# Performance work log

Hardware: AMD Instinct MI355X
Metric: run time of the kernel (lower is better)

## Reference

```python
import jax, jax.numpy as jnp
import numpy as np

NUM_HEADS = 12
HIDDEN = 768
HEAD = HIDDEN // NUM_HEADS
SCALE = HIDDEN ** (-0.5)  # NB: module scales by hidden_dim**-0.5, not head_size**-0.5


def setup_inputs() -> dict:
    key = jax.random.key(0)
    ks = jax.random.split(key, 8)
    B, N = 16, 512
    std = HIDDEN ** (-0.5)
    return {
        "x": jax.random.normal(ks[0], (B, N, HIDDEN), dtype=jnp.float32),
        "encoding_bias": jax.random.normal(ks[1], (B, N, N), dtype=jnp.float32),
        "Wq": jax.random.normal(ks[2], (HIDDEN, HIDDEN), dtype=jnp.float32) * std,
        "Wk": jax.random.normal(ks[3], (HIDDEN, HIDDEN), dtype=jnp.float32) * std,
        "Wv": jax.random.normal(ks[4], (HIDDEN, HIDDEN), dtype=jnp.float32) * std,
        "bv": jax.random.normal(ks[5], (HIDDEN,), dtype=jnp.float32) * 0.01,
        "Wo": jax.random.normal(ks[6], (HIDDEN, HIDDEN), dtype=jnp.float32) * std,
        "bo": jax.random.normal(ks[7], (HIDDEN,), dtype=jnp.float32) * 0.01,
    }


def reference(x, encoding_bias, Wq, Wk, Wv, bv, Wo, bo):
    B, N, _ = x.shape
    # torch nn.Linear: y = x @ W.T (+ b)
    q = (x @ Wq.T).reshape(B, N, NUM_HEADS, HEAD)
    k = (x @ Wk.T).reshape(B, N, NUM_HEADS, HEAD)
    v = (x @ Wv.T + bv).reshape(B, N, NUM_HEADS, HEAD)
    # scores: [B, H, N, N] with additive graph bias broadcast over heads
    a = jnp.einsum("bnhd,bmhd->bhnm", q, k) * SCALE + encoding_bias[:, None, :, :]
    # data-dependent pad mask: rows whose scores are identically zero
    pad_mask = jnp.all(a == 0, axis=-1)  # [B, H, N]
    a = jnp.where(pad_mask[..., None], -jnp.inf, a)
    a = jax.nn.softmax(a, axis=-1)
    a = jnp.nan_to_num(a)  # all -inf rows -> NaN -> 0
    o = jnp.einsum("bhnm,bmhd->bnhd", a, v).reshape(B, N, HIDDEN)
    # dropout is identity in eval mode
    return o @ Wo.T + bo
```

## Files before the change

### kernel.cpp

```cpp
#include <hip/hip_runtime.h>
#include <stdint.h>

typedef unsigned short u16;
typedef unsigned int u32;
typedef __bf16 bf16x8 __attribute__((ext_vector_type(8)));
typedef float f32x4 __attribute__((ext_vector_type(4)));

#define NH 12
#define HD 64
#define SEQ 512
#define BATCH 16
#define HID 768
#define SCALE_Q 0.03608439182435161f

__device__ __forceinline__ u16 f2bf(float f) {
    u32 u = __builtin_bit_cast(u32, f);
    u32 r = (u + 0x7FFFu + ((u >> 16) & 1u)) >> 16;
    return (u16)r;
}
__device__ __forceinline__ float bf2f(u16 h) {
    return __builtin_bit_cast(float, (u32)h << 16);
}

__device__ __forceinline__ void gl2lds16(const u16* g, u16* lds_base) {
    __builtin_amdgcn_global_load_lds(
        (const __attribute__((address_space(1))) u32*)g,
        (__attribute__((address_space(3))) u32*)lds_base, 16, 0, 0);
}

#define NXB 6144
#define NEB 4096
#define NWB 576
__global__ void cvt_all(const float* __restrict__ x, const float* __restrict__ eb,
                        const float* __restrict__ w0, const float* __restrict__ w1,
                        const float* __restrict__ w2, const float* __restrict__ w3,
                        u16* __restrict__ dst) {
    int b = blockIdx.x;
    const float* s; int sb;
    if (b < NXB) { s = x; sb = 0; }
    else if (b < NXB + NEB) { s = eb; sb = NXB; }
    else if (b < NXB + NEB + NWB) { s = w0; sb = NXB + NEB; }
    else if (b < NXB + NEB + 2 * NWB) { s = w1; sb = NXB + NEB + NWB; }
    else if (b < NXB + NEB + 3 * NWB) { s = w2; sb = NXB + NEB + 2 * NWB; }
    else { s = w3; sb = NXB + NEB + 3 * NWB; }
    int li = (b - sb) * 1024 + threadIdx.x * 4;
    float4 v = *(const float4*)(s + li);
    ushort4 o;
    o.x = f2bf(v.x); o.y = f2bf(v.y); o.z = f2bf(v.z); o.w = f2bf(v.w);
    *(ushort4*)(dst + (size_t)b * 1024 + threadIdx.x * 4) = o;
}

__device__ __forceinline__ void stage_gemm(
    const u16* __restrict__ Ag, const u16* __restrict__ Bg, int k0,
    u16* As, u16* Bs, int r0, int q0, int r1, int q1, int w)
{
    gl2lds16(Ag + (size_t)r0 * HID + k0 + q0, As + w * 512);
    gl2lds16(Ag + (size_t)r1 * HID + k0 + q1, As + 2048 + w * 512);
    gl2lds16(Bg + (size_t)r0 * HID + k0 + q0, Bs + w * 512);
    gl2lds16(Bg + (size_t)r1 * HID + k0 + q1, Bs + 2048 + w * 512);
}

__device__ __forceinline__ void gemm_mainloop(
    const u16* __restrict__ Ag, const u16* __restrict__ Bg,
    u16 (*As)[128 * 32], u16 (*Bs)[128 * 32], f32x4 (&acc)[4][4])
{
    const int tid = threadIdx.x;
    const int l = tid & 63, w = tid >> 6;
    const int wm = w & 1, wn = w >> 1;
    const int lr = l & 15, lg = l >> 4;

    const int c0 = tid, c1 = tid + 256;
    const int r0 = c0 >> 2, q0 = (((c0 & 3) ^ ((r0 >> 1) & 3)) * 8);
    const int r1 = c1 >> 2, q1 = (((c1 & 3) ^ ((r1 >> 1) & 3)) * 8);

    const int sA = (lg ^ ((lr >> 1) & 3)) * 8;

    stage_gemm(Ag, Bg, 0, As[0], Bs[0], r0, q0, r1, q1, w);
    stage_gemm(Ag, Bg, 32, As[1], Bs[1], r0, q0, r1, q1, w);

    int cur = 0;
    for (int i = 0; i < 24; i++) {
        if (i < 23)
            asm volatile("s_waitcnt vmcnt(4) lgkmcnt(0)" ::: "memory");
        else
            asm volatile("s_waitcnt vmcnt(0) lgkmcnt(0)" ::: "memory");
        __builtin_amdgcn_s_barrier();
        __builtin_amdgcn_sched_barrier(0);

        int nxt = cur + 2; if (nxt >= 3) nxt -= 3;
        if (i < 22)
            stage_gemm(Ag, Bg, (i + 2) * 32, As[nxt], Bs[nxt], r0, q0, r1, q1, w);

        bf16x8 af[4], bfr[4];
#pragma unroll
        for (int mi = 0; mi < 4; mi++)
            af[mi] = *(const bf16x8*)(As[cur] + (wm * 64 + mi * 16 + lr) * 32 + sA);
#pragma unroll
        for (int ni = 0; ni < 4; ni++)
            bfr[ni] = *(const bf16x8*)(Bs[cur] + (wn * 64 + ni * 16 + lr) * 32 + sA);
#pragma unroll
        for (int mi = 0; mi < 4; mi++)
#pragma unroll
            for (int ni = 0; ni < 4; ni++)
                acc[mi][ni] = __builtin_amdgcn_mfma_f32_16x16x32_bf16(af[mi], bfr[ni], acc[mi][ni], 0, 0, 0);

        cur += 1; if (cur >= 3) cur -= 3;
    }
}

__global__ __launch_bounds__(256, 3) void gemm_qkv(
    const u16* __restrict__ xb, const u16* __restrict__ wq,
    const u16* __restrict__ wk, const u16* __restrict__ wv,
    const float* __restrict__ bv,
    u16* __restrict__ qtb, u16* __restrict__ kb, u16* __restrict__ vtb)
{
    __shared__ __align__(16) u16 As[3][128 * 32];
    __shared__ __align__(16) u16 Bs[3][128 * 32];
    const int tid = threadIdx.x;
    const int l = tid & 63, w = tid >> 6;
    const int wm = w & 1, wn = w >> 1;
    const int lr = l & 15, lg = l >> 4;
    const int mt = blockIdx.x, nt = blockIdx.y, z = blockIdx.z;

    const u16* Bw = (z == 0) ? wq : (z == 1) ? wk : wv;
    const u16* Ag = xb + (size_t)(mt * 128) * HID;
    const u16* Bg = Bw + (size_t)(nt * 128) * HID;

    f32x4 acc[4][4] = {};
    gemm_mainloop(Ag, Bg, As, Bs, acc);

    const float sc = (z == 0) ? SCALE_Q : 1.0f;
#pragma unroll
    for (int mi = 0; mi < 4; mi++) {
#pragma unroll
        for (int ni = 0; ni < 4; ni++) {
            const int jg = nt * 128 + wn * 64 + ni * 16 + lr;
            const int h = jg >> 6, d = jg & 63;
            const int i0 = mt * 128 + wm * 64 + mi * 16 + lg * 4;
            const int b = i0 >> 9, n0 = i0 & 511;
            if (z == 1) {
#pragma unroll
                for (int r2 = 0; r2 < 4; r2++)
                    kb[((size_t)(b * NH + h) * SEQ + n0 + r2) * HD + d] = f2bf(acc[mi][ni][r2]);
            } else {
                float bb = (z == 2) ? bv[jg] : 0.0f;
                ushort4 pk;
                pk.x = f2bf(fmaf(acc[mi][ni][0], sc, bb));
                pk.y = f2bf(fmaf(acc[mi][ni][1], sc, bb));
                pk.z = f2bf(fmaf(acc[mi][ni][2], sc, bb));
                pk.w = f2bf(fmaf(acc[mi][ni][3], sc, bb));
                u16* O = (z == 0) ? qtb : vtb;
                *(ushort4*)(O + ((size_t)(b * NH + h) * HD + d) * SEQ + n0) = pk;
            }
        }
    }
}

__global__ __launch_bounds__(256, 3) void gemm_out(
    const u16* __restrict__ A, const u16* __restrict__ wo,
    const float* __restrict__ bo, float* __restrict__ Cout)
{
    __shared__ __align__(16) u16 As[3][128 * 32];
    __shared__ __align__(16) u16 Bs[3][128 * 32];
    const int tid = threadIdx.x;
    const int l = tid & 63, w = tid >> 6;
    const int wm = w & 1, wn = w >> 1;
    const int lr = l & 15, lg = l >> 4;
    const int mt = blockIdx.x, nt = blockIdx.y;

    const u16* Ag = A + (size_t)(mt * 128) * HID;
    const u16* Bg = wo + (size_t)(nt * 128) * HID;

    f32x4 acc[4][4] = {};
    gemm_mainloop(Ag, Bg, As, Bs, acc);

#pragma unroll
    for (int mi = 0; mi < 4; mi++) {
#pragma unroll
        for (int ni = 0; ni < 4; ni++) {
            const int jg = nt * 128 + wn * 64 + ni * 16 + lr;
            float bb = bo[jg];
#pragma unroll
            for (int r2 = 0; r2 < 4; r2++) {
                int ig = mt * 128 + wm * 64 + mi * 16 + lg * 4 + r2;
                Cout[(size_t)ig * HID + jg] = acc[mi][ni][r2] + bb;
            }
        }
    }
}

__device__ __forceinline__ void stage_kv(
    const u16* __restrict__ Kg, const u16* __restrict__ Vg, int mt0,
    u16* Ksb, u16* Vsb, int kr0, int kc0, int kr1, int kc1, int w)
{
    gl2lds16(Kg + (size_t)(mt0 + kr0) * HD + kc0 * 8, Ksb + w * 512);
    gl2lds16(Kg + (size_t)(mt0 + kr1) * HD + kc1 * 8, Ksb + 2048 + w * 512);
    gl2lds16(Vg + (size_t)kr0 * SEQ + mt0 + kc0 * 8, Vsb + w * 512);
    gl2lds16(Vg + (size_t)kr1 * SEQ + mt0 + kc1 * 8, Vsb + 2048 + w * 512);
}

__global__ __launch_bounds__(256, 4) void attn_kernel(
    const u16* __restrict__ qtb, const u16* __restrict__ kb, const u16* __restrict__ vtb,
    const u16* __restrict__ ebb, u16* __restrict__ ob)
{
    __shared__ __align__(16) u16 Ks[2][64 * 64];
    __shared__ __align__(16) u16 Vs[2][64 * 64];
    __shared__ __align__(16) u16 Ps[4][16 * 64];

    const int tid = threadIdx.x;
    const int l = tid & 63, w = tid >> 6;
    const int lr = l & 15, lg = l >> 4;
    const int h = blockIdx.x, qt = blockIdx.y, b = blockIdx.z;
    const int bh = b * NH + h;
    const int qrow0 = qt * 64 + w * 16;

    const u16* Kg = kb + (size_t)bh * SEQ * HD;
    const u16* Vg = vtb + (size_t)bh * HD * SEQ;
    const u16* Eg = ebb + ((size_t)b * SEQ + qrow0 + lg * 4) * SEQ;

    const int p0 = tid, p1 = tid + 256;
    const int kr0 = p0 >> 3, kc0 = (p0 & 7) ^ (kr0 & 7);
    const int kr1 = p1 >> 3, kc1 = (p1 & 7) ^ (kr1 & 7);

    stage_kv(Kg, Vg, 0, Ks[0], Vs[0], kr0, kc0, kr1, kc1, w);

    const u16* Qg = qtb + (size_t)bh * HD * SEQ + qrow0 + lr;
    bf16x8 qf0, qf1;
#pragma unroll
    for (int j = 0; j < 8; j++) {
        qf0[j] = __builtin_bit_cast(__bf16, Qg[(size_t)(lg * 8 + j) * SEQ]);
        qf1[j] = __builtin_bit_cast(__bf16, Qg[(size_t)(lg * 8 + j + 32) * SEQ]);
    }

    bf16x8 ones;
#pragma unroll
    for (int j = 0; j < 8; j++) ones[j] = __builtin_bit_cast(__bf16, (u16)0x3F80);

    f32x4 oacc[4] = {};
    f32x4 lacc = {};
    float amax[4] = {0.f, 0.f, 0.f, 0.f};

    for (int t = 0; t < 8; t++) {
        const int cur = t & 1;
        const int mt0 = t * 64;
        __syncthreads();

        u16 bl[4][4];
#pragma unroll
        for (int mi = 0; mi < 4; mi++)
#pragma unroll
            for (int r = 0; r < 4; r++)
                bl[mi][r] = Eg[(size_t)r * SEQ + mt0 + mi * 16 + lr];

        if (t < 7)
            stage_kv(Kg, Vg, mt0 + 64, Ks[cur ^ 1], Vs[cur ^ 1], kr0, kc0, kr1, kc1, w);

        float sm[4][4];
#pragma unroll
        for (int mi = 0; mi < 4; mi++) {
            const int row = mi * 16 + lr;
            bf16x8 kf0 = *(const bf16x8*)(Ks[cur] + row * 64 + ((lg ^ (row & 7)) * 8));
            bf16x8 kf1 = *(const bf16x8*)(Ks[cur] + row * 64 + (((4 + lg) ^ (row & 7)) * 8));
            f32x4 s;
#pragma unroll
            for (int r = 0; r < 4; r++) s[r] = bf2f(bl[mi][r]);
            s = __builtin_amdgcn_mfma_f32_16x16x32_bf16(qf0, kf0, s, 0, 0, 0);
            s = __builtin_amdgcn_mfma_f32_16x16x32_bf16(qf1, kf1, s, 0, 0, 0);
#pragma unroll
            for (int r = 0; r < 4; r++) {
                float sv = s[r];
                amax[r] = fmaxf(amax[r], fabsf(sv));
                sm[mi][r] = __expf(sv);
            }
        }

        u16* Pw = Ps[w];
#pragma unroll
        for (int mi = 0; mi < 4; mi++)
#pragma unroll
            for (int r = 0; r < 4; r++) {
                const int q = lg * 4 + r;
                const int chunk = mi * 2 + (lr >> 3);
                Pw[q * 64 + ((chunk ^ (q & 7)) * 8) + (lr & 7)] = f2bf(sm[mi][r]);
            }

#pragma unroll
        for (int ks = 0; ks < 2; ks++) {
            bf16x8 pf = *(const bf16x8*)(Pw + lr * 64 + (((ks * 4 + lg) ^ (lr & 7)) * 8));
#pragma unroll
            for (int di = 0; di < 4; di++) {
                const int row = di * 16 + lr;
                bf16x8 vf = *(const bf16x8*)(Vs[cur] + row * 64 + (((ks * 4 + lg) ^ (row & 7)) * 8));
                oacc[di] = __builtin_amdgcn_mfma_f32_16x16x32_bf16(pf, vf, oacc[di], 0, 0, 0);
            }
            lacc = __builtin_amdgcn_mfma_f32_16x16x32_bf16(pf, ones, lacc, 0, 0, 0);
        }
    }

#pragma unroll
    for (int r = 0; r < 4; r++) {
        float am = amax[r];
        am = fmaxf(am, __shfl_xor(am, 1));
        am = fmaxf(am, __shfl_xor(am, 2));
        am = fmaxf(am, __shfl_xor(am, 4));
        am = fmaxf(am, __shfl_xor(am, 8));
        float inv = (am > 0.f) ? (1.0f / lacc[r]) : 0.0f;
        int n = qrow0 + lg * 4 + r;
        u16* orow = ob + ((size_t)b * SEQ + n) * HID + h * HD;
#pragma unroll
        for (int di = 0; di < 4; di++)
            orow[di * 16 + lr] = f2bf(oacc[di][r] * inv);
    }
}

extern "C" void kernel_launch(void* const* d_in, const int* in_sizes, int n_in,
                              void* d_out, int out_size, void* d_ws, size_t ws_size,
                              hipStream_t stream) {
    (void)in_sizes; (void)n_in; (void)out_size; (void)ws_size;
    const float* x  = (const float*)d_in[0];
    const float* eb = (const float*)d_in[1];
    const float* Wq = (const float*)d_in[2];
    const float* Wk = (const float*)d_in[3];
    const float* Wv = (const float*)d_in[4];
    const float* bv = (const float*)d_in[5];
    const float* Wo = (const float*)d_in[6];
    const float* bo = (const float*)d_in[7];
    float* out = (float*)d_out;

    const int NX = BATCH * SEQ * HID;
    const int NW = HID * HID;
    const int NE = BATCH * SEQ * SEQ;
    u16* ws   = (u16*)d_ws;
    u16* xb   = ws;
    u16* ebb  = xb + NX;
    u16* wqb  = ebb + NE;
    u16* wkb  = wqb + NW;
    u16* wvb  = wkb + NW;
    u16* wob  = wvb + NW;
    u16* qtb  = wob + NW;
    u16* kb   = qtb + NX;
    u16* vtb  = kb + NX;
    u16* obuf = vtb + NX;

    cvt_all<<<NXB + NEB + 4 * NWB, 256, 0, stream>>>(x, eb, Wq, Wk, Wv, Wo, ws);

    gemm_qkv<<<dim3(64, 6, 3), 256, 0, stream>>>(xb, wqb, wkb, wvb, bv, qtb, kb, vtb);

    attn_kernel<<<dim3(NH, 8, BATCH), 256, 0, stream>>>(qtb, kb, vtb, ebb, obuf);

    gemm_out<<<dim3(64, 6), 256, 0, stream>>>(obuf, wob, bo, out);
}
```

Measured before the change: 204.2 us.

## Widen QKV GEMM tile to 128x256 and remap attention blocks per XCD

```diff
diff --git a/kernel.cpp b/kernel.cpp
--- a/kernel.cpp
+++ b/kernel.cpp
@@ -50,38 +50,50 @@
     *(ushort4*)(dst + (size_t)b * 1024 + threadIdx.x * 4) = o;
 }
 
-__device__ __forceinline__ void stage_gemm(
+__device__ __forceinline__ void stage_gemm256(
     const u16* __restrict__ Ag, const u16* __restrict__ Bg, int k0,
-    u16* As, u16* Bs, int r0, int q0, int r1, int q1, int w)
-{
-    gl2lds16(Ag + (size_t)r0 * HID + k0 + q0, As + w * 512);
-    gl2lds16(Ag + (size_t)r1 * HID + k0 + q1, As + 2048 + w * 512);
-    gl2lds16(Bg + (size_t)r0 * HID + k0 + q0, Bs + w * 512);
-    gl2lds16(Bg + (size_t)r1 * HID + k0 + q1, Bs + 2048 + w * 512);
-}
-
-__device__ __forceinline__ void gemm_mainloop(
+    u16* As, u16* Bs,
+    int ra0, int qa0, int ra1, int qa1,
+    int rb0, int qb0, int rb1, int qb1,
+    int rb2, int qb2, int rb3, int qb3, int w)
+{
+    gl2lds16(Ag + (size_t)ra0 * HID + k0 + qa0, As + w * 512);
+    gl2lds16(Ag + (size_t)ra1 * HID + k0 + qa1, As + 2048 + w * 512);
+    gl2lds16(Bg + (size_t)rb0 * HID + k0 + qb0, Bs + w * 512);
+    gl2lds16(Bg + (size_t)rb1 * HID + k0 + qb1, Bs + 2048 + w * 512);
+    gl2lds16(Bg + (size_t)rb2 * HID + k0 + qb2, Bs + 4096 + w * 512);
+    gl2lds16(Bg + (size_t)rb3 * HID + k0 + qb3, Bs + 6144 + w * 512);
+}
+
+__device__ __forceinline__ void gemm_mainloop256(
     const u16* __restrict__ Ag, const u16* __restrict__ Bg,
-    u16 (*As)[128 * 32], u16 (*Bs)[128 * 32], f32x4 (&acc)[4][4])
+    u16 (*As)[128 * 32], u16 (*Bs)[256 * 32], f32x4 (&acc)[4][8])
 {
     const int tid = threadIdx.x;
     const int l = tid & 63, w = tid >> 6;
     const int wm = w & 1, wn = w >> 1;
     const int lr = l & 15, lg = l >> 4;
 
-    const int c0 = tid, c1 = tid + 256;
-    const int r0 = c0 >> 2, q0 = (((c0 & 3) ^ ((r0 >> 1) & 3)) * 8);
-    const int r1 = c1 >> 2, q1 = (((c1 & 3) ^ ((r1 >> 1) & 3)) * 8);
+    const int ca0 = tid, ca1 = tid + 256;
+    const int ra0 = ca0 >> 2, qa0 = (((ca0 & 3) ^ ((ra0 >> 1) & 3)) * 8);
+    const int ra1 = ca1 >> 2, qa1 = (((ca1 & 3) ^ ((ra1 >> 1) & 3)) * 8);
+    const int cb0 = tid, cb1 = tid + 256, cb2 = tid + 512, cb3 = tid + 768;
+    const int rb0 = cb0 >> 2, qb0 = (((cb0 & 3) ^ ((rb0 >> 1) & 3)) * 8);
+    const int rb1 = cb1 >> 2, qb1 = (((cb1 & 3) ^ ((rb1 >> 1) & 3)) * 8);
+    const int rb2 = cb2 >> 2, qb2 = (((cb2 & 3) ^ ((rb2 >> 1) & 3)) * 8);
+    const int rb3 = cb3 >> 2, qb3 = (((cb3 & 3) ^ ((rb3 >> 1) & 3)) * 8);
 
     const int sA = (lg ^ ((lr >> 1) & 3)) * 8;
 
-    stage_gemm(Ag, Bg, 0, As[0], Bs[0], r0, q0, r1, q1, w);
-    stage_gemm(Ag, Bg, 32, As[1], Bs[1], r0, q0, r1, q1, w);
+    stage_gemm256(Ag, Bg, 0, As[0], Bs[0], ra0, qa0, ra1, qa1,
+                  rb0, qb0, rb1, qb1, rb2, qb2, rb3, qb3, w);
+    stage_gemm256(Ag, Bg, 32, As[1], Bs[1], ra0, qa0, ra1, qa1,
+                  rb0, qb0, rb1, qb1, rb2, qb2, rb3, qb3, w);
 
     int cur = 0;
     for (int i = 0; i < 24; i++) {
         if (i < 23)
-            asm volatile("s_waitcnt vmcnt(4) lgkmcnt(0)" ::: "memory");
+            asm volatile("s_waitcnt vmcnt(6) lgkmcnt(0)" ::: "memory");
         else
             asm volatile("s_waitcnt vmcnt(0) lgkmcnt(0)" ::: "memory");
         __builtin_amdgcn_s_barrier();
@@ -89,33 +101,34 @@
 
         int nxt = cur + 2; if (nxt >= 3) nxt -= 3;
         if (i < 22)
-            stage_gemm(Ag, Bg, (i + 2) * 32, As[nxt], Bs[nxt], r0, q0, r1, q1, w);
-
-        bf16x8 af[4], bfr[4];
+            stage_gemm256(Ag, Bg, (i + 2) * 32, As[nxt], Bs[nxt], ra0, qa0, ra1, qa1,
+                          rb0, qb0, rb1, qb1, rb2, qb2, rb3, qb3, w);
+
+        bf16x8 af[4], bfr[8];
 #pragma unroll
         for (int mi = 0; mi < 4; mi++)
             af[mi] = *(const bf16x8*)(As[cur] + (wm * 64 + mi * 16 + lr) * 32 + sA);
 #pragma unroll
-        for (int ni = 0; ni < 4; ni++)
-            bfr[ni] = *(const bf16x8*)(Bs[cur] + (wn * 64 + ni * 16 + lr) * 32 + sA);
-#pragma unroll
-        for (int mi = 0; mi < 4; mi++)
-#pragma unroll
-            for (int ni = 0; ni < 4; ni++)
+        for (int ni = 0; ni < 8; ni++)
+            bfr[ni] = *(const bf16x8*)(Bs[cur] + (wn * 128 + ni * 16 + lr) * 32 + sA);
+#pragma unroll
+        for (int mi = 0; mi < 4; mi++)
+#pragma unroll
+            for (int ni = 0; ni < 8; ni++)
                 acc[mi][ni] = __builtin_amdgcn_mfma_f32_16x16x32_bf16(af[mi], bfr[ni], acc[mi][ni], 0, 0, 0);
 
         cur += 1; if (cur >= 3) cur -= 3;
     }
 }
 
-__global__ __launch_bounds__(256, 3) void gemm_qkv(
+__global__ __launch_bounds__(256, 2) void gemm_qkv(
     const u16* __restrict__ xb, const u16* __restrict__ wq,
     const u16* __restrict__ wk, const u16* __restrict__ wv,
     const float* __restrict__ bv,
     u16* __restrict__ qtb, u16* __restrict__ kb, u16* __restrict__ vtb)
 {
     __shared__ __align__(16) u16 As[3][128 * 32];
-    __shared__ __align__(16) u16 Bs[3][128 * 32];
+    __shared__ __align__(16) u16 Bs[3][256 * 32];
     const int tid = threadIdx.x;
     const int l = tid & 63, w = tid >> 6;
     const int wm = w & 1, wn = w >> 1;
@@ -124,17 +137,17 @@
 
     const u16* Bw = (z == 0) ? wq : (z == 1) ? wk : wv;
     const u16* Ag = xb + (size_t)(mt * 128) * HID;
-    const u16* Bg = Bw + (size_t)(nt * 128) * HID;
-
-    f32x4 acc[4][4] = {};
-    gemm_mainloop(Ag, Bg, As, Bs, acc);
+    const u16* Bg = Bw + (size_t)(nt * 256) * HID;
+
+    f32x4 acc[4][8] = {};
+    gemm_mainloop256(Ag, Bg, As, Bs, acc);
 
     const float sc = (z == 0) ? SCALE_Q : 1.0f;
 #pragma unroll
     for (int mi = 0; mi < 4; mi++) {
 #pragma unroll
-        for (int ni = 0; ni < 4; ni++) {
-            const int jg = nt * 128 + wn * 64 + ni * 16 + lr;
+        for (int ni = 0; ni < 8; ni++) {
+            const int jg = nt * 256 + wn * 128 + ni * 16 + lr;
             const int h = jg >> 6, d = jg & 63;
             const int i0 = mt * 128 + wm * 64 + mi * 16 + lg * 4;
             const int b = i0 >> 9, n0 = i0 & 511;
@@ -156,6 +169,64 @@
     }
 }
 
+__device__ __forceinline__ void stage_gemm(
+    const u16* __restrict__ Ag, const u16* __restrict__ Bg, int k0,
+    u16* As, u16* Bs, int r0, int q0, int r1, int q1, int w)
+{
+    gl2lds16(Ag + (size_t)r0 * HID + k0 + q0, As + w * 512);
+    gl2lds16(Ag + (size_t)r1 * HID + k0 + q1, As + 2048 + w * 512);
+    gl2lds16(Bg + (size_t)r0 * HID + k0 + q0, Bs + w * 512);
+    gl2lds16(Bg + (size_t)r1 * HID + k0 + q1, Bs + 2048 + w * 512);
+}
+
+__device__ __forceinline__ void gemm_mainloop(
+    const u16* __restrict__ Ag, const u16* __restrict__ Bg,
+    u16 (*As)[128 * 32], u16 (*Bs)[128 * 32], f32x4 (&acc)[4][4])
+{
+    const int tid = threadIdx.x;
+    const int l = tid & 63, w = tid >> 6;
+    const int wm = w & 1, wn = w >> 1;
+    const int lr = l & 15, lg = l >> 4;
+
+    const int c0 = tid, c1 = tid + 256;
+    const int r0 = c0 >> 2, q0 = (((c0 & 3) ^ ((r0 >> 1) & 3)) * 8);
+    const int r1 = c1 >> 2, q1 = (((c1 & 3) ^ ((r1 >> 1) & 3)) * 8);
+
+    const int sA = (lg ^ ((lr >> 1) & 3)) * 8;
+
+    stage_gemm(Ag, Bg, 0, As[0], Bs[0], r0, q0, r1, q1, w);
+    stage_gemm(Ag, Bg, 32, As[1], Bs[1], r0, q0, r1, q1, w);
+
+    int cur = 0;
+    for (int i = 0; i < 24; i++) {
+        if (i < 23)
+            asm volatile("s_waitcnt vmcnt(4) lgkmcnt(0)" ::: "memory");
+        else
+            asm volatile("s_waitcnt vmcnt(0) lgkmcnt(0)" ::: "memory");
+        __builtin_amdgcn_s_barrier();
+        __builtin_amdgcn_sched_barrier(0);
+
+        int nxt = cur + 2; if (nxt >= 3) nxt -= 3;
+        if (i < 22)
+            stage_gemm(Ag, Bg, (i + 2) * 32, As[nxt], Bs[nxt], r0, q0, r1, q1, w);
+
+        bf16x8 af[4], bfr[4];
+#pragma unroll
+        for (int mi = 0; mi < 4; mi++)
+            af[mi] = *(const bf16x8*)(As[cur] + (wm * 64 + mi * 16 + lr) * 32 + sA);
+#pragma unroll
+        for (int ni = 0; ni < 4; ni++)
+            bfr[ni] = *(const bf16x8*)(Bs[cur] + (wn * 64 + ni * 16 + lr) * 32 + sA);
+#pragma unroll
+        for (int mi = 0; mi < 4; mi++)
+#pragma unroll
+            for (int ni = 0; ni < 4; ni++)
+                acc[mi][ni] = __builtin_amdgcn_mfma_f32_16x16x32_bf16(af[mi], bfr[ni], acc[mi][ni], 0, 0, 0);
+
+        cur += 1; if (cur >= 3) cur -= 3;
+    }
+}
+
 __global__ __launch_bounds__(256, 3) void gemm_out(
     const u16* __restrict__ A, const u16* __restrict__ wo,
     const float* __restrict__ bo, float* __restrict__ Cout)
@@ -210,7 +281,13 @@
     const int tid = threadIdx.x;
     const int l = tid & 63, w = tid >> 6;
     const int lr = l & 15, lg = l >> 4;
-    const int h = blockIdx.x, qt = blockIdx.y, b = blockIdx.z;
+
+    const int L = blockIdx.x;
+    const int xcd = L & 7, s = L >> 3;
+    const int b = xcd * 2 + (s / 96);
+    const int s2 = s % 96;
+    const int h = s2 >> 3, qt = s2 & 7;
+
     const int bh = b * NH + h;
     const int qrow0 = qt * 64 + w * 16;
 
@@ -344,9 +421,9 @@
 
     cvt_all<<<NXB + NEB + 4 * NWB, 256, 0, stream>>>(x, eb, Wq, Wk, Wv, Wo, ws);
 
-    gemm_qkv<<<dim3(64, 6, 3), 256, 0, stream>>>(xb, wqb, wkb, wvb, bv, qtb, kb, vtb);
-
-    attn_kernel<<<dim3(NH, 8, BATCH), 256, 0, stream>>>(qtb, kb, vtb, ebb, obuf);
+    gemm_qkv<<<dim3(64, 3, 3), 256, 0, stream>>>(xb, wqb, wkb, wvb, bv, qtb, kb, vtb);
+
+    attn_kernel<<<1536, 256, 0, stream>>>(qtb, kb, vtb, ebb, obuf);
 
     gemm_out<<<dim3(64, 6), 256, 0, stream>>>(obuf, wob, bo, out);
 }
```

New measurement: 221.8 us. 1.09x slower.

## Process two query tiles per attention block and remap blocks to XCDs

Applied to the files above, without the earlier changes.

```diff
diff --git a/kernel.cpp b/kernel.cpp
--- a/kernel.cpp
+++ b/kernel.cpp
@@ -166,7 +166,11 @@
     const int l = tid & 63, w = tid >> 6;
     const int wm = w & 1, wn = w >> 1;
     const int lr = l & 15, lg = l >> 4;
-    const int mt = blockIdx.x, nt = blockIdx.y;
+
+    const int L = blockIdx.x;
+    const int xcd = L & 7, s = L >> 3;
+    const int nt = s >> 3;
+    const int mt = xcd * 8 + (s & 7);
 
     const u16* Ag = A + (size_t)(mt * 128) * HID;
     const u16* Bg = wo + (size_t)(nt * 128) * HID;
@@ -199,24 +203,31 @@
     gl2lds16(Vg + (size_t)kr1 * SEQ + mt0 + kc1 * 8, Vsb + 2048 + w * 512);
 }
 
-__global__ __launch_bounds__(256, 4) void attn_kernel(
+__global__ __launch_bounds__(256, 3) void attn_kernel(
     const u16* __restrict__ qtb, const u16* __restrict__ kb, const u16* __restrict__ vtb,
     const u16* __restrict__ ebb, u16* __restrict__ ob)
 {
     __shared__ __align__(16) u16 Ks[2][64 * 64];
     __shared__ __align__(16) u16 Vs[2][64 * 64];
-    __shared__ __align__(16) u16 Ps[4][16 * 64];
+    __shared__ __align__(16) u16 Ps[8][16 * 64];
 
     const int tid = threadIdx.x;
     const int l = tid & 63, w = tid >> 6;
     const int lr = l & 15, lg = l >> 4;
-    const int h = blockIdx.x, qt = blockIdx.y, b = blockIdx.z;
+
+    const int L = blockIdx.x;
+    const int xcd = L & 7, s = L >> 3;
+    const int b = xcd * 2 + (s / 48);
+    const int s2 = s % 48;
+    const int h = s2 >> 2, qt = s2 & 3;
+
     const int bh = b * NH + h;
-    const int qrow0 = qt * 64 + w * 16;
+    const int qrow0 = qt * 128 + w * 16;
 
     const u16* Kg = kb + (size_t)bh * SEQ * HD;
     const u16* Vg = vtb + (size_t)bh * HD * SEQ;
-    const u16* Eg = ebb + ((size_t)b * SEQ + qrow0 + lg * 4) * SEQ;
+    const u16* Eg0 = ebb + ((size_t)b * SEQ + qrow0 + lg * 4) * SEQ;
+    const u16* Eg1 = Eg0 + (size_t)64 * SEQ;
 
     const int p0 = tid, p1 = tid + 256;
     const int kr0 = p0 >> 3, kc0 = (p0 & 7) ^ (kr0 & 7);
@@ -225,91 +236,114 @@
     stage_kv(Kg, Vg, 0, Ks[0], Vs[0], kr0, kc0, kr1, kc1, w);
 
     const u16* Qg = qtb + (size_t)bh * HD * SEQ + qrow0 + lr;
-    bf16x8 qf0, qf1;
+    bf16x8 qA0, qA1, qB0, qB1;
 #pragma unroll
     for (int j = 0; j < 8; j++) {
-        qf0[j] = __builtin_bit_cast(__bf16, Qg[(size_t)(lg * 8 + j) * SEQ]);
-        qf1[j] = __builtin_bit_cast(__bf16, Qg[(size_t)(lg * 8 + j + 32) * SEQ]);
+        qA0[j] = __builtin_bit_cast(__bf16, Qg[(size_t)(lg * 8 + j) * SEQ]);
+        qA1[j] = __builtin_bit_cast(__bf16, Qg[(size_t)(lg * 8 + j + 32) * SEQ]);
+        qB0[j] = __builtin_bit_cast(__bf16, Qg[(size_t)(lg * 8 + j) * SEQ + 64]);
+        qB1[j] = __builtin_bit_cast(__bf16, Qg[(size_t)(lg * 8 + j + 32) * SEQ + 64]);
     }
 
     bf16x8 ones;
 #pragma unroll
     for (int j = 0; j < 8; j++) ones[j] = __builtin_bit_cast(__bf16, (u16)0x3F80);
 
-    f32x4 oacc[4] = {};
-    f32x4 lacc = {};
-    float amax[4] = {0.f, 0.f, 0.f, 0.f};
+    f32x4 oacc0[4] = {}, oacc1[4] = {};
+    f32x4 lacc0 = {}, lacc1 = {};
+    float amax0[4] = {0.f, 0.f, 0.f, 0.f};
+    float amax1[4] = {0.f, 0.f, 0.f, 0.f};
+    u16* Pw0 = Ps[w];
+    u16* Pw1 = Ps[4 + w];
 
     for (int t = 0; t < 8; t++) {
         const int cur = t & 1;
         const int mt0 = t * 64;
         __syncthreads();
 
-        u16 bl[4][4];
+        u16 bl0[4][4], bl1[4][4];
 #pragma unroll
         for (int mi = 0; mi < 4; mi++)
 #pragma unroll
-            for (int r = 0; r < 4; r++)
-                bl[mi][r] = Eg[(size_t)r * SEQ + mt0 + mi * 16 + lr];
+            for (int r = 0; r < 4; r++) {
+                bl0[mi][r] = Eg0[(size_t)r * SEQ + mt0 + mi * 16 + lr];
+                bl1[mi][r] = Eg1[(size_t)r * SEQ + mt0 + mi * 16 + lr];
+            }
 
         if (t < 7)
             stage_kv(Kg, Vg, mt0 + 64, Ks[cur ^ 1], Vs[cur ^ 1], kr0, kc0, kr1, kc1, w);
 
-        float sm[4][4];
+        float sm0[4][4], sm1[4][4];
 #pragma unroll
         for (int mi = 0; mi < 4; mi++) {
             const int row = mi * 16 + lr;
             bf16x8 kf0 = *(const bf16x8*)(Ks[cur] + row * 64 + ((lg ^ (row & 7)) * 8));
             bf16x8 kf1 = *(const bf16x8*)(Ks[cur] + row * 64 + (((4 + lg) ^ (row & 7)) * 8));
-            f32x4 s;
-#pragma unroll
-            for (int r = 0; r < 4; r++) s[r] = bf2f(bl[mi][r]);
-            s = __builtin_amdgcn_mfma_f32_16x16x32_bf16(qf0, kf0, s, 0, 0, 0);
-            s = __builtin_amdgcn_mfma_f32_16x16x32_bf16(qf1, kf1, s, 0, 0, 0);
+            f32x4 s0, s1;
+#pragma unroll
+            for (int r = 0; r < 4; r++) { s0[r] = bf2f(bl0[mi][r]); s1[r] = bf2f(bl1[mi][r]); }
+            s0 = __builtin_amdgcn_mfma_f32_16x16x32_bf16(qA0, kf0, s0, 0, 0, 0);
+            s0 = __builtin_amdgcn_mfma_f32_16x16x32_bf16(qA1, kf1, s0, 0, 0, 0);
+            s1 = __builtin_amdgcn_mfma_f32_16x16x32_bf16(qB0, kf0, s1, 0, 0, 0);
+            s1 = __builtin_amdgcn_mfma_f32_16x16x32_bf16(qB1, kf1, s1, 0, 0, 0);
 #pragma unroll
             for (int r = 0; r < 4; r++) {
-                float sv = s[r];
-                amax[r] = fmaxf(amax[r], fabsf(sv));
-                sm[mi][r] = __expf(sv);
-            }
-        }
-
-        u16* Pw = Ps[w];
+                float a = s0[r], c = s1[r];
+                amax0[r] = fmaxf(amax0[r], fabsf(a));
+                amax1[r] = fmaxf(amax1[r], fabsf(c));
+                sm0[mi][r] = __expf(a);
+                sm1[mi][r] = __expf(c);
+            }
+        }
+
 #pragma unroll
         for (int mi = 0; mi < 4; mi++)
 #pragma unroll
             for (int r = 0; r < 4; r++) {
                 const int q = lg * 4 + r;
                 const int chunk = mi * 2 + (lr >> 3);
-                Pw[q * 64 + ((chunk ^ (q & 7)) * 8) + (lr & 7)] = f2bf(sm[mi][r]);
+                const int off = q * 64 + ((chunk ^ (q & 7)) * 8) + (lr & 7);
+                Pw0[off] = f2bf(sm0[mi][r]);
+                Pw1[off] = f2bf(sm1[mi][r]);
             }
 
 #pragma unroll
         for (int ks = 0; ks < 2; ks++) {
-            bf16x8 pf = *(const bf16x8*)(Pw + lr * 64 + (((ks * 4 + lg) ^ (lr & 7)) * 8));
+            bf16x8 pf0 = *(const bf16x8*)(Pw0 + lr * 64 + (((ks * 4 + lg) ^ (lr & 7)) * 8));
+            bf16x8 pf1 = *(const bf16x8*)(Pw1 + lr * 64 + (((ks * 4 + lg) ^ (lr & 7)) * 8));
 #pragma unroll
             for (int di = 0; di < 4; di++) {
                 const int row = di * 16 + lr;
                 bf16x8 vf = *(const bf16x8*)(Vs[cur] + row * 64 + (((ks * 4 + lg) ^ (row & 7)) * 8));
-                oacc[di] = __builtin_amdgcn_mfma_f32_16x16x32_bf16(pf, vf, oacc[di], 0, 0, 0);
-            }
-            lacc = __builtin_amdgcn_mfma_f32_16x16x32_bf16(pf, ones, lacc, 0, 0, 0);
+                oacc0[di] = __builtin_amdgcn_mfma_f32_16x16x32_bf16(pf0, vf, oacc0[di], 0, 0, 0);
+                oacc1[di] = __builtin_amdgcn_mfma_f32_16x16x32_bf16(pf1, vf, oacc1[di], 0, 0, 0);
+            }
+            lacc0 = __builtin_amdgcn_mfma_f32_16x16x32_bf16(pf0, ones, lacc0, 0, 0, 0);
+            lacc1 = __builtin_amdgcn_mfma_f32_16x16x32_bf16(pf1, ones, lacc1, 0, 0, 0);
         }
     }
 
 #pragma unroll
     for (int r = 0; r < 4; r++) {
-        float am = amax[r];
-        am = fmaxf(am, __shfl_xor(am, 1));
-        am = fmaxf(am, __shfl_xor(am, 2));
-        am = fmaxf(am, __shfl_xor(am, 4));
-        am = fmaxf(am, __shfl_xor(am, 8));
-        float inv = (am > 0.f) ? (1.0f / lacc[r]) : 0.0f;
-        int n = qrow0 + lg * 4 + r;
-        u16* orow = ob + ((size_t)b * SEQ + n) * HID + h * HD;
-#pragma unroll
-        for (int di = 0; di < 4; di++)
-            orow[di * 16 + lr] = f2bf(oacc[di][r] * inv);
+        float am0 = amax0[r], am1 = amax1[r];
+        am0 = fmaxf(am0, __shfl_xor(am0, 1));
+        am0 = fmaxf(am0, __shfl_xor(am0, 2));
+        am0 = fmaxf(am0, __shfl_xor(am0, 4));
+        am0 = fmaxf(am0, __shfl_xor(am0, 8));
+        am1 = fmaxf(am1, __shfl_xor(am1, 1));
+        am1 = fmaxf(am1, __shfl_xor(am1, 2));
+        am1 = fmaxf(am1, __shfl_xor(am1, 4));
+        am1 = fmaxf(am1, __shfl_xor(am1, 8));
+        float inv0 = (am0 > 0.f) ? (1.0f / lacc0[r]) : 0.0f;
+        float inv1 = (am1 > 0.f) ? (1.0f / lacc1[r]) : 0.0f;
+        int n0 = qrow0 + lg * 4 + r;
+        u16* orow0 = ob + ((size_t)b * SEQ + n0) * HID + h * HD;
+        u16* orow1 = ob + ((size_t)b * SEQ + n0 + 64) * HID + h * HD;
+#pragma unroll
+        for (int di = 0; di < 4; di++) {
+            orow0[di * 16 + lr] = f2bf(oacc0[di][r] * inv0);
+            orow1[di * 16 + lr] = f2bf(oacc1[di][r] * inv1);
+        }
     }
 }
 
@@ -346,7 +380,7 @@
 
     gemm_qkv<<<dim3(64, 6, 3), 256, 0, stream>>>(xb, wqb, wkb, wvb, bv, qtb, kb, vtb);
 
-    attn_kernel<<<dim3(NH, 8, BATCH), 256, 0, stream>>>(qtb, kb, vtb, ebb, obuf);
-
-    gemm_out<<<dim3(64, 6), 256, 0, stream>>>(obuf, wob, bo, out);
-}
+    attn_kernel<<<768, 256, 0, stream>>>(qtb, kb, vtb, ebb, obuf);
+
+    gemm_out<<<384, 256, 0, stream>>>(obuf, wob, bo, out);
+}
```

New measurement: 198.0 us (median of 2 runs). 1.03x faster.
